# Performance work log

Hardware: AMD Instinct MI355X
Metric: run time of the kernel (lower is better)

## Reference

```python
import math
import jax, jax.numpy as jnp
import numpy as np

HIDDEN = 256
COND = 512
N_HEADS = 4


def _rope_freqs(seq_len, dim, theta=10000.0):
    inv = 1.0 / (theta ** (jnp.arange(0, dim, 2, dtype=jnp.float32) / dim))
    f = jnp.arange(seq_len, dtype=jnp.float32)[:, None] * inv[None, :]  # [t, dim/2]
    return jnp.concatenate([f, f], axis=-1)  # [t, dim]


def _rotate_half(x):
    x1, x2 = jnp.split(x, 2, axis=-1)
    return jnp.concatenate([-x2, x1], axis=-1)


def _apply_rope(pos, t):
    # pos: [T, c] broadcast over [b, h, T, c]
    return t * jnp.cos(pos) + _rotate_half(t) * jnp.sin(pos)


def _conv1(w, b, x):
    # 1x1 Conv1d: w [out, in], x [b, in, t]
    return jnp.einsum('oi,bit->bot', w, x) + b[None, :, None]


def setup_inputs() -> dict:
    key = jax.random.key(0)
    ks = jax.random.split(key, 12)
    B, Tt, Ts = 16, 2048, 512
    s = 0.02
    return {
        'x': jax.random.normal(ks[0], (B, HIDDEN, Tt), jnp.float32),
        'x_mask': jnp.ones((B, 1, Tt), jnp.float32),
        'cond_latent': jax.random.normal(ks[1], (B, COND, Ts), jnp.float32),
        'cond_mask': jnp.ones((B, 1, Ts), jnp.float32),
        'w_cond': jax.random.normal(ks[2], (HIDDEN, COND), jnp.float32) * s,
        'b_cond': jnp.zeros((HIDDEN,), jnp.float32),
        'wq': jax.random.normal(ks[3], (HIDDEN, HIDDEN), jnp.float32) * s,
        'bq': jnp.zeros((HIDDEN,), jnp.float32),
        'wk': jax.random.normal(ks[4], (HIDDEN, HIDDEN), jnp.float32) * s,
        'bk': jnp.zeros((HIDDEN,), jnp.float32),
        'wv': jax.random.normal(ks[5], (HIDDEN, HIDDEN), jnp.float32) * s,
        'bv': jnp.zeros((HIDDEN,), jnp.float32),
        'wo': jax.random.normal(ks[6], (HIDDEN, HIDDEN), jnp.float32) * s,
        'bo': jnp.zeros((HIDDEN,), jnp.float32),
        'w_film': jax.random.normal(ks[7], (2 * HIDDEN, HIDDEN), jnp.float32) * s,
        'b_film': jnp.zeros((2 * HIDDEN,), jnp.float32),
    }


def reference(x, x_mask, cond_latent, cond_mask,
              w_cond, b_cond, wq, bq, wk, bk, wv, bv, wo, bo, w_film, b_film):
    c = _conv1(w_cond, b_cond, cond_latent)          # [b, C, Ts]
    q = _conv1(wq, bq, x)                            # [b, C, Tt]
    k = _conv1(wk, bk, c)
    v = _conv1(wv, bv, c)

    B, C, Tt = q.shape
    Ts = k.shape[2]
    h = N_HEADS
    kc = C // h

    def split_heads(t):
        # [b, (h c), T] -> [b, h, T, c]
        return t.reshape(B, h, kc, t.shape[-1]).transpose(0, 1, 3, 2)

    q, k, v = split_heads(q), split_heads(k), split_heads(v)

    q = _apply_rope(_rope_freqs(Tt, kc), q)
    k = _apply_rope(_rope_freqs(Ts, kc), k)

    scores = jnp.einsum('bhtc,bhsc->bhts', q, k) / math.sqrt(kc)  # [b, h, Tt, Ts]
    attn_mask = cond_mask[:, :, None, :] * x_mask[:, :, :, None]  # [b, 1, Tt, Ts]
    scores = jnp.where(attn_mask == 0, jnp.float32(-1e4), scores)
    p = jax.nn.softmax(scores, axis=-1)  # dropout is identity at eval
    out = jnp.einsum('bhts,bhsc->bhtc', p, v)
    out = out.transpose(0, 1, 3, 2).reshape(B, C, Tt)  # [b, (h c), Tt]

    y = _conv1(wo, bo, out)                 # [b, C, Tt]
    gb = _conv1(w_film, b_film, y)          # [b, 2C, Tt]
    gamma, beta = jnp.split(gb, 2, axis=1)
    return (x * gamma + beta) * x_mask
```

## Files before the change

kernel.cpp:

```cpp
#include <hip/hip_runtime.h>
#include <math.h>

#define NB 16
#define CH 256
#define NH 4
#define KC 64
#define TTT 2048
#define TSS 512

typedef __attribute__((ext_vector_type(8))) short bf16x8;
typedef __attribute__((ext_vector_type(4))) float f32x4;

__device__ inline short f2bf(float x) {
  unsigned u = __float_as_uint(x);
  u += 0x7fffu + ((u >> 16) & 1u);
  return (short)(u >> 16);
}
__device__ inline unsigned pack2bf(float a, float b) {
  return (unsigned)(unsigned short)f2bf(a) | ((unsigned)(unsigned short)f2bf(b) << 16);
}

__device__ inline void fast_sincos_rev(float rev, float* sn, float* cs) {
  float fr = rev - truncf(rev);
#if __has_builtin(__builtin_amdgcn_sinf)
  *sn = __builtin_amdgcn_sinf(fr);
  *cs = __builtin_amdgcn_cosf(fr);
#else
  float ang = fr * 6.28318530717958648f;
  *sn = __sinf(ang);
  *cs = __cosf(ang);
#endif
}

#define INV2PI 0.15915494309189535f
#define ROPE_C 0.28782313662425572f

template <int TN, int NOUT>
__global__ __launch_bounds__(256) void gemm_v2(
    const float* __restrict__ W0, const float* __restrict__ b0,
    const float* __restrict__ W1, const float* __restrict__ b1,
    const float* __restrict__ X, float* __restrict__ Y0, float* __restrict__ Y1,
    int K, int T) {
  constexpr int TT = 16 * TN;
  constexpr int TQ = TT / 4;
  constexpr int PB = (32 * TQ) / 256;
  const int t0 = blockIdx.x * TT;
  const int m0 = blockIdx.y * 64;
  const int b  = blockIdx.z;
  const int tid = threadIdx.x;
  const int tx = tid & 15, ty = tid >> 4;

  __shared__ float As[NOUT][32][68];
  __shared__ float Bs[32][TT + 4];

  const float* Xb = X + (size_t)b * K * T;
  float acc[NOUT][4][TN];
#pragma unroll
  for (int n = 0; n < NOUT; ++n)
#pragma unroll
    for (int i = 0; i < 4; ++i)
#pragma unroll
      for (int u = 0; u < TN; ++u) acc[n][i][u] = 0.f;

  const int am = tid >> 2, akq = tid & 3;

  for (int k0 = 0; k0 < K; k0 += 32) {
#pragma unroll
    for (int n = 0; n < NOUT; ++n) {
      const float* Wn = (n == 0) ? W0 : W1;
      float4 a0 = *(const float4*)&Wn[(size_t)(m0 + am) * K + k0 + 4 * akq];
      float4 a1 = *(const float4*)&Wn[(size_t)(m0 + am) * K + k0 + 16 + 4 * akq];
      As[n][4 * akq + 0][am] = a0.x; As[n][4 * akq + 1][am] = a0.y;
      As[n][4 * akq + 2][am] = a0.z; As[n][4 * akq + 3][am] = a0.w;
      As[n][16 + 4 * akq + 0][am] = a1.x; As[n][16 + 4 * akq + 1][am] = a1.y;
      As[n][16 + 4 * akq + 2][am] = a1.z; As[n][16 + 4 * akq + 3][am] = a1.w;
    }
#pragma unroll
    for (int p = 0; p < PB; ++p) {
      int idx = tid + p * 256;
      int t4 = idx & (TQ - 1), k = idx / TQ;
      *(float4*)&Bs[k][4 * t4] = *(const float4*)&Xb[(size_t)(k0 + k) * T + t0 + 4 * t4];
    }
    __syncthreads();
#pragma unroll
    for (int kk = 0; kk < 32; ++kk) {
      float4 av[NOUT];
#pragma unroll
      for (int n = 0; n < NOUT; ++n) av[n] = *(const float4*)&As[n][kk][4 * ty];
      float4 bv[TN / 4];
#pragma unroll
      for (int g = 0; g < TN / 4; ++g) bv[g] = *(const float4*)&Bs[kk][4 * tx + 64 * g];
#pragma unroll
      for (int n = 0; n < NOUT; ++n) {
        const float a4[4] = {av[n].x, av[n].y, av[n].z, av[n].w};
#pragma unroll
        for (int i = 0; i < 4; ++i)
#pragma unroll
          for (int g = 0; g < TN / 4; ++g) {
            acc[n][i][4 * g + 0] += a4[i] * bv[g].x;
            acc[n][i][4 * g + 1] += a4[i] * bv[g].y;
            acc[n][i][4 * g + 2] += a4[i] * bv[g].z;
            acc[n][i][4 * g + 3] += a4[i] * bv[g].w;
          }
      }
    }
    __syncthreads();
  }
#pragma unroll
  for (int n = 0; n < NOUT; ++n) {
    float* Yn = (n == 0) ? Y0 : Y1;
    const float* bn = (n == 0) ? b0 : b1;
#pragma unroll
    for (int i = 0; i < 4; ++i) {
      int row = m0 + 4 * ty + i;
      float bi = bn[row];
#pragma unroll
      for (int g = 0; g < TN / 4; ++g) {
        float4 ov;
        ov.x = acc[n][i][4 * g + 0] + bi; ov.y = acc[n][i][4 * g + 1] + bi;
        ov.z = acc[n][i][4 * g + 2] + bi; ov.w = acc[n][i][4 * g + 3] + bi;
        *(float4*)&Yn[((size_t)b * 256 + row) * T + t0 + 4 * tx + 64 * g] = ov;
      }
    }
  }
}

__global__ __launch_bounds__(256, 2) void gemm_q_mfma(
    const short* __restrict__ wqbf, const float* __restrict__ bq,
    const float* __restrict__ X, short* __restrict__ qbf) {
  const int t0 = blockIdx.x * 64;
  const int b  = blockIdx.y;
  const int tid = threadIdx.x;
  const int w = tid >> 6, lane = tid & 63;
  const int quad = lane >> 4, l15 = lane & 15;

  __shared__ __align__(16) char smem[72704];
  float* Bsq = (float*)smem;
  float* Ep  = (float*)smem;

  const float* xb = X + (size_t)b * CH * TTT + t0;
#pragma unroll
  for (int p = 0; p < 16; ++p) {
    int idx = tid + p * 256;
    int t4 = idx & 15, k = idx >> 4;
    int swz = ((k >> 3) & 3) * 16;
    *(float4*)&Bsq[k * 68 + ((4 * t4) ^ swz)] =
        *(const float4*)&xb[(size_t)k * TTT + 4 * t4];
  }
  __syncthreads();

  const int mbase = w * 64;
  f32x4 acc[4][4];
#pragma unroll
  for (int mf = 0; mf < 4; ++mf)
#pragma unroll
    for (int nt = 0; nt < 4; ++nt) acc[mf][nt] = (f32x4){0.f, 0.f, 0.f, 0.f};

#pragma unroll
  for (int k0 = 0; k0 < 256; k0 += 32) {
    bf16x8 bfr[4];
#pragma unroll
    for (int nt = 0; nt < 4; ++nt) {
      int col = (nt * 16 + l15) ^ (quad * 16);
      bf16x8 f;
#pragma unroll
      for (int j = 0; j < 8; ++j)
        f[j] = f2bf(Bsq[(k0 + quad * 8 + j) * 68 + col]);
      bfr[nt] = f;
    }
#pragma unroll
    for (int mf = 0; mf < 4; ++mf) {
      bf16x8 af = *(const bf16x8*)&wqbf[(size_t)(mbase + mf * 16 + l15) * 256 + k0 + quad * 8];
#pragma unroll
      for (int nt = 0; nt < 4; ++nt)
        acc[mf][nt] = __builtin_amdgcn_mfma_f32_16x16x32_bf16(af, bfr[nt], acc[mf][nt], 0, 0, 0);
    }
  }
  __syncthreads();

#pragma unroll
  for (int mf = 0; mf < 4; ++mf)
#pragma unroll
    for (int r = 0; r < 4; ++r) {
      int row = mbase + mf * 16 + quad * 4 + r;
      float bi = bq[row];
#pragma unroll
      for (int nt = 0; nt < 4; ++nt)
        Ep[row * 71 + nt * 16 + l15] = acc[mf][nt][r] + bi;
    }
  __syncthreads();

  const int tt = tid >> 2, cb = tid & 3;
  float sn[8], cs[8];
  const float tg = (float)(t0 + tt);
#pragma unroll
  for (int e = 0; e < 8; ++e) {
    float invr = __expf(-(float)(cb * 8 + e) * ROPE_C) * INV2PI;
    fast_sincos_rev(tg * invr, &sn[e], &cs[e]);
  }
#pragma unroll
  for (int hh = 0; hh < 4; ++hh) {
    float oa[8], oc[8];
#pragma unroll
    for (int e = 0; e < 8; ++e) {
      int j = cb * 8 + e;
      float a = Ep[(hh * 64 + j) * 71 + tt];
      float c = Ep[(hh * 64 + j + 32) * 71 + tt];
      oa[e] = a * cs[e] - c * sn[e];
      oc[e] = c * cs[e] + a * sn[e];
    }
    short* dst = qbf + ((size_t)(b * NH + hh) * TTT + t0 + tt) * 64 + cb * 8;
    *(uint4*)dst = make_uint4(pack2bf(oa[0], oa[1]), pack2bf(oa[2], oa[3]),
                              pack2bf(oa[4], oa[5]), pack2bf(oa[6], oa[7]));
    *(uint4*)(dst + 32) = make_uint4(pack2bf(oc[0], oc[1]), pack2bf(oc[2], oc[3]),
                                     pack2bf(oc[4], oc[5]), pack2bf(oc[6], oc[7]));
  }
}

__global__ __launch_bounds__(256, 2) void gemm_kv_mfma(
    const short* __restrict__ wkvbf,
    const float* __restrict__ bk2, const float* __restrict__ bv2,
    const float* __restrict__ X, short* __restrict__ kbf, short* __restrict__ vbf) {
  const int t0 = blockIdx.x * 64;
  const int hh = blockIdx.y;
  const int b  = blockIdx.z;
  const int tid = threadIdx.x;
  const int w = tid >> 6, lane = tid & 63;
  const int quad = lane >> 4, l15 = lane & 15;

  __shared__ __align__(16) char smem[69632];
  short* Ls = (short*)smem;
  float* Kv = (float*)smem;

  const float* Xb = X + (size_t)b * 512 * TSS + t0;
#pragma unroll
  for (int p = 0; p < 32; ++p) {
    int idx = tid + p * 256;
    int s4 = idx & 15, k = idx >> 4;
    float4 v = *(const float4*)&Xb[(size_t)k * TSS + 4 * s4];
    uint2 w2 = make_uint2(pack2bf(v.x, v.y), pack2bf(v.z, v.w));
    *(uint2*)&Ls[k * 68 + 4 * s4] = w2;
  }
  __syncthreads();

  const int isV = w >> 1;
  const int wbase = (w & 1) * 32;
  const short* wbf = wkvbf + (size_t)(isV * 256 + hh * 64 + wbase) * 512;
  const float* bias = isV ? bv2 : bk2;

  f32x4 acc[2][4];
#pragma unroll
  for (int mf = 0; mf < 2; ++mf)
#pragma unroll
    for (int nt = 0; nt < 4; ++nt) acc[mf][nt] = (f32x4){0.f, 0.f, 0.f, 0.f};

#pragma unroll
  for (int k0 = 0; k0 < 512; k0 += 32) {
    bf16x8 bfr[4];
#pragma unroll
    for (int nt = 0; nt < 4; ++nt) {
      int s = nt * 16 + l15;
      bf16x8 f;
#pragma unroll
      for (int j = 0; j < 8; ++j)
        f[j] = Ls[(k0 + quad * 8 + j) * 68 + s];
      bfr[nt] = f;
    }
#pragma unroll
    for (int mf = 0; mf < 2; ++mf) {
      bf16x8 af = *(const bf16x8*)&wbf[(size_t)(mf * 16 + l15) * 512 + k0 + quad * 8];
#pragma unroll
      for (int nt = 0; nt < 4; ++nt)
        acc[mf][nt] = __builtin_amdgcn_mfma_f32_16x16x32_bf16(af, bfr[nt], acc[mf][nt], 0, 0, 0);
    }
  }
  __syncthreads();

#pragma unroll
  for (int mf = 0; mf < 2; ++mf)
#pragma unroll
    for (int r = 0; r < 4; ++r) {
      int lr = wbase + mf * 16 + quad * 4 + r;
      int ro = isV * 64 + lr;
      float bi = bias[hh * 64 + lr];
#pragma unroll
      for (int nt = 0; nt < 4; ++nt)
        Kv[ro * 68 + nt * 16 + l15] = acc[mf][nt][r] + bi;
    }
  __syncthreads();

  const int bh = b * NH + hh;

#pragma unroll
  for (int p = 0; p < 4; ++p) {
    int idx = tid + p * 256;
    int s4 = idx & 15, ch = idx >> 4;
    float4 v = *(const float4*)&Kv[(64 + ch) * 68 + 4 * s4];
    uint2 w2 = make_uint2(pack2bf(v.x, v.y), pack2bf(v.z, v.w));
    *(uint2*)&vbf[((size_t)bh * KC + ch) * TSS + t0 + 4 * s4] = w2;
  }

  {
    int s = tid >> 2, g = tid & 3;
    float sg = (float)(t0 + s);
    unsigned ow[8];
#pragma unroll
    for (int hlf = 0; hlf < 8; ++hlf) {
      int ch = g * 16 + hlf * 2;
      float o2[2];
#pragma unroll
      for (int q = 0; q < 2; ++q) {
        int c = ch + q;
        int j = c & 31;
        float invr = __expf(-(float)j * ROPE_C) * INV2PI;
        float snv, csv;
        fast_sincos_rev(sg * invr, &snv, &csv);
        float a = Kv[c * 68 + s];
        float pv = Kv[(c ^ 32) * 68 + s];
        o2[q] = (c < 32) ? (a * csv - pv * snv) : (a * csv + pv * snv);
      }
      ow[hlf] = pack2bf(o2[0], o2[1]);
    }
    short* dst = kbf + ((size_t)bh * TSS + t0 + s) * 64 + g * 16;
    *(uint4*)dst = make_uint4(ow[0], ow[1], ow[2], ow[3]);
    *(uint4*)(dst + 8) = make_uint4(ow[4], ow[5], ow[6], ow[7]);
  }
}

__global__ __launch_bounds__(256) void bias_fold(
    const float* __restrict__ wk, const float* __restrict__ bk,
    const float* __restrict__ wv, const float* __restrict__ bv,
    const float* __restrict__ bcond,
    const float* __restrict__ wfilm, const float* __restrict__ bo,
    const float* __restrict__ bfilm,
    float* __restrict__ bk2, float* __restrict__ bv2, float* __restrict__ bf2) {
  int g = blockIdx.x * 256 + threadIdx.x;
  if (g < 256) {
    float s = bk[g];
    for (int k = 0; k < 256; ++k) s += wk[g * 256 + k] * bcond[k];
    bk2[g] = s;
  } else if (g < 512) {
    int m = g - 256;
    float s = bv[m];
    for (int k = 0; k < 256; ++k) s += wv[m * 256 + k] * bcond[k];
    bv2[m] = s;
  } else if (g < 1024) {
    int m = g - 512;
    float s = bfilm[m];
    for (int k = 0; k < 256; ++k) s += wfilm[m * 256 + k] * bo[k];
    bf2[m] = s;
  }
}

__global__ __launch_bounds__(256) void cvt_bf16(
    const float* __restrict__ src, short* __restrict__ dst, int n) {
  int i = (blockIdx.x * 256 + threadIdx.x) * 8;
  if (i < n) {
    float4 a = *(const float4*)&src[i];
    float4 c = *(const float4*)&src[i + 4];
    uint4 w;
    w.x = pack2bf(a.x, a.y); w.y = pack2bf(a.z, a.w);
    w.z = pack2bf(c.x, c.y); w.w = pack2bf(c.z, c.w);
    *(uint4*)&dst[i] = w;
  }
}

__global__ __launch_bounds__(256, 3) void attn_mfma(
    const short* __restrict__ qbf, const short* __restrict__ kbf,
    const short* __restrict__ vbf, const float* __restrict__ cond_mask,
    short* __restrict__ obuf) {
  const int t0 = blockIdx.x * 64;
  const int h = blockIdx.y, b = blockIdx.z;
  const int bh = b * NH + h;
  const int tid = threadIdx.x;
  const int w = tid >> 6, lane = tid & 63;
  const int quad = lane >> 4, l15 = lane & 15;

  __shared__ __align__(16) char smem[49152];
  short* Ks = (short*)smem;
  short* Vs = (short*)(smem + 16384);
  short* Ps = (short*)(smem + 32768);

  const short* qb = qbf + ((size_t)bh * TTT + t0) * 64;
  const int trow_l = w * 16 + l15;
  bf16x8 qf0 = *(const bf16x8*)&qb[(size_t)trow_l * 64 + quad * 8];
  bf16x8 qf1 = *(const bf16x8*)&qb[(size_t)trow_l * 64 + 32 + quad * 8];

  f32x4 acc_o[4];
#pragma unroll
  for (int n = 0; n < 4; ++n) acc_o[n] = (f32x4){0.f, 0.f, 0.f, 0.f};
  float den[4] = {0.f, 0.f, 0.f, 0.f};

  const float* cm = cond_mask + (size_t)b * TSS;
  const short* kbase = kbf + (size_t)bh * TSS * 64;
  const short* vbase = vbf + (size_t)bh * KC * TSS;

  for (int s0 = 0; s0 < TSS; s0 += 128) {
    __syncthreads();
#pragma unroll
    for (int p = 0; p < 4; ++p) {
      int idx = tid + p * 256;
      int blk = idx & 7, sr = idx >> 3;
      *(uint4*)&Ks[sr * 64 + 8 * (blk ^ (sr & 7))] =
          *(const uint4*)&kbase[(size_t)(s0 + sr) * 64 + 8 * blk];
    }
#pragma unroll
    for (int p = 0; p < 4; ++p) {
      int idx = tid + p * 256;
      int blk = idx & 15, ch = idx >> 4;
      *(uint4*)&Vs[ch * 128 + 8 * (blk ^ (ch & 7))] =
          *(const uint4*)&vbase[(size_t)ch * TSS + s0 + 8 * blk];
    }
    __syncthreads();

#pragma unroll
    for (int n0 = 0; n0 < 8; ++n0) {
      int srow = n0 * 16 + l15;
      bf16x8 kf0 = *(const bf16x8*)&Ks[srow * 64 + 8 * (quad ^ (srow & 7))];
      bf16x8 kf1 = *(const bf16x8*)&Ks[srow * 64 + 8 * ((4 + quad) ^ (srow & 7))];
      f32x4 acc = (f32x4){0.f, 0.f, 0.f, 0.f};
      acc = __builtin_amdgcn_mfma_f32_16x16x32_bf16(qf0, kf0, acc, 0, 0, 0);
      acc = __builtin_amdgcn_mfma_f32_16x16x32_bf16(qf1, kf1, acc, 0, 0, 0);
      float mk = (cm[s0 + srow] != 0.f) ? 1.f : 0.f;
      int sblk = n0 * 2 + (l15 >> 3);
      int slow = l15 & 7;
#pragma unroll
      for (int r = 0; r < 4; ++r) {
        float e = __expf(acc[r] * 0.125f) * mk;
        den[r] += e;
        int trow = w * 16 + quad * 4 + r;
        Ps[trow * 128 + 8 * (sblk ^ (trow & 7)) + slow] = f2bf(e);
      }
    }

    {
      int trow = w * 16 + l15;
#pragma unroll
      for (int kt = 0; kt < 4; ++kt) {
        bf16x8 pf = *(const bf16x8*)&Ps[trow * 128 + 8 * ((kt * 4 + quad) ^ (trow & 7))];
#pragma unroll
        for (int n0 = 0; n0 < 4; ++n0) {
          int ch = n0 * 16 + l15;
          bf16x8 vf = *(const bf16x8*)&Vs[ch * 128 + 8 * ((kt * 4 + quad) ^ (ch & 7))];
          acc_o[n0] = __builtin_amdgcn_mfma_f32_16x16x32_bf16(pf, vf, acc_o[n0], 0, 0, 0);
        }
      }
    }
  }

  float rd[4];
#pragma unroll
  for (int r = 0; r < 4; ++r) {
    float d = den[r];
#pragma unroll
    for (int off = 1; off < 16; off <<= 1) d += __shfl_xor(d, off, 16);
    rd[r] = 1.f / fmaxf(d, 1e-30f);
  }

  __syncthreads();
  short* Os = (short*)smem;
#pragma unroll
  for (int n0 = 0; n0 < 4; ++n0)
#pragma unroll
    for (int r = 0; r < 4; ++r) {
      int ch = n0 * 16 + l15;
      int trow = w * 16 + quad * 4 + r;
      Os[trow * 64 + ch] = f2bf(acc_o[n0][r] * rd[r]);
    }
  __syncthreads();

  short* ob = obuf + ((size_t)b * TTT + t0) * CH + h * KC;
#pragma unroll
  for (int p = 0; p < 2; ++p) {
    int idx = tid + p * 256;
    int t = idx >> 3, c8 = idx & 7;
    *(uint4*)&ob[(size_t)t * CH + c8 * 8] = *(const uint4*)&Os[t * 64 + c8 * 8];
  }
}

__global__ __launch_bounds__(256) void film_mfma(
    const short* __restrict__ wfbf, const float* __restrict__ bf2,
    const short* __restrict__ ybf, const float* __restrict__ X,
    const float* __restrict__ xmask, float* __restrict__ out) {
  const int t0 = blockIdx.x * 64;
  const int b = blockIdx.y;
  const int tid = threadIdx.x;
  const int w = tid >> 6, lane = tid & 63;
  const int quad = lane >> 4, l15 = lane & 15;

  __shared__ __align__(16) short Ys[64 * 256];

  const short* yb = ybf + ((size_t)b * TTT + t0) * CH;
#pragma unroll
  for (int p = 0; p < 8; ++p) {
    int idx = tid + p * 256;
    int cb = idx & 31, tr = idx >> 5;
    *(uint4*)&Ys[tr * 256 + 8 * (cb ^ (tr & 7))] =
        *(const uint4*)&yb[(size_t)tr * CH + 8 * cb];
  }
  __syncthreads();

  const int mbase = w * 64;
  f32x4 accg[4][4], accb[4][4];
#pragma unroll
  for (int mf = 0; mf < 4; ++mf)
#pragma unroll
    for (int nt = 0; nt < 4; ++nt) {
      accg[mf][nt] = (f32x4){0.f, 0.f, 0.f, 0.f};
      accb[mf][nt] = (f32x4){0.f, 0.f, 0.f, 0.f};
    }

#pragma unroll
  for (int k0 = 0; k0 < 256; k0 += 32) {
    const int cb0 = (k0 >> 3) + quad;
    bf16x8 bfr[4];
#pragma unroll
    for (int nt = 0; nt < 4; ++nt) {
      int tr = nt * 16 + l15;
      bfr[nt] = *(const bf16x8*)&Ys[tr * 256 + 8 * (cb0 ^ (tr & 7))];
    }
#pragma unroll
    for (int mf = 0; mf < 4; ++mf) {
      int rowg = mbase + mf * 16 + l15;
      bf16x8 ag = *(const bf16x8*)&wfbf[(size_t)rowg * 256 + k0 + quad * 8];
      bf16x8 ab = *(const bf16x8*)&wfbf[(size_t)(256 + rowg) * 256 + k0 + quad * 8];
#pragma unroll
      for (int nt = 0; nt < 4; ++nt) {
        accg[mf][nt] = __builtin_amdgcn_mfma_f32_16x16x32_bf16(ag, bfr[nt], accg[mf][nt], 0, 0, 0);
        accb[mf][nt] = __builtin_amdgcn_mfma_f32_16x16x32_bf16(ab, bfr[nt], accb[mf][nt], 0, 0, 0);
      }
    }
  }

  const float* xb = X + (size_t)b * CH * TTT + t0;
  const float* xm = xmask + (size_t)b * TTT + t0;
  float* ob = out + (size_t)b * CH * TTT + t0;
  float xmv[4];
#pragma unroll
  for (int nt = 0; nt < 4; ++nt) xmv[nt] = xm[nt * 16 + l15];

#pragma unroll
  for (int mf = 0; mf < 4; ++mf) {
#pragma unroll
    for (int r = 0; r < 4; ++r) {
      int row = mbase + mf * 16 + quad * 4 + r;
      float bg = bf2[row];
      float bb = bf2[256 + row];
#pragma unroll
      for (int nt = 0; nt < 4; ++nt) {
        int t = nt * 16 + l15;
        float g  = accg[mf][nt][r] + bg;
        float bt = accb[mf][nt][r] + bb;
        float xv = xb[(size_t)row * TTT + t];
        ob[(size_t)row * TTT + t] = (xv * g + bt) * xmv[nt];
      }
    }
  }
}

extern "C" void kernel_launch(void* const* d_in, const int* in_sizes, int n_in,
                              void* d_out, int out_size, void* d_ws, size_t ws_size,
                              hipStream_t stream) {
  const float* x           = (const float*)d_in[0];
  const float* x_mask      = (const float*)d_in[1];
  const float* cond_latent = (const float*)d_in[2];
  const float* cond_mask   = (const float*)d_in[3];
  const float* w_cond      = (const float*)d_in[4];
  const float* b_cond      = (const float*)d_in[5];
  const float* wq          = (const float*)d_in[6];
  const float* bq          = (const float*)d_in[7];
  const float* wk          = (const float*)d_in[8];
  const float* bk          = (const float*)d_in[9];
  const float* wv          = (const float*)d_in[10];
  const float* bv          = (const float*)d_in[11];
  const float* wo          = (const float*)d_in[12];
  const float* bo          = (const float*)d_in[13];
  const float* w_film      = (const float*)d_in[14];
  const float* b_film      = (const float*)d_in[15];
  float* out = (float*)d_out;

  float* ws = (float*)d_ws;
  float* k_buf = ws;
  float* v_buf = k_buf + 2097152;
  float* wk2   = v_buf + 2097152;
  float* wv2   = wk2 + 131072;
  float* wf2   = wv2 + 131072;
  float* bk2   = wf2 + 131072;
  float* bv2   = bk2 + 256;
  float* bf2   = bv2 + 256;
  float* zbuf  = bf2 + 512;
  short* k_bf  = (short*)(zbuf + 512);
  short* v_bf  = k_bf + 2097152;
  short* wf2bf = v_bf + 2097152;
  short* q_bf  = wf2bf + 131072;
  short* wq_bf = q_bf + 8388608;
  short* wkv_bf = wq_bf + 65536;
  short* o_bf  = (short*)k_buf;

  dim3 blk(256);

  hipMemsetAsync(zbuf, 0, 512 * sizeof(float), stream);

  cvt_bf16<<<dim3(32), blk, 0, stream>>>(wq, wq_bf, 65536);
  gemm_v2<4, 2><<<dim3(8, 4, 1), blk, 0, stream>>>(
      wk, zbuf, wv, zbuf, w_cond, wk2, wv2, 256, 512);
  gemm_v2<4, 1><<<dim3(4, 8, 1), blk, 0, stream>>>(
      w_film, zbuf, nullptr, nullptr, wo, wf2, nullptr, 256, 256);
  cvt_bf16<<<dim3(128), blk, 0, stream>>>(wk2, wkv_bf, 262144);
  cvt_bf16<<<dim3(64), blk, 0, stream>>>(wf2, wf2bf, 131072);
  bias_fold<<<dim3(4), blk, 0, stream>>>(wk, bk, wv, bv, b_cond,
                                         w_film, bo, b_film, bk2, bv2, bf2);

  gemm_q_mfma<<<dim3(32, 16), blk, 0, stream>>>(wq_bf, bq, x, q_bf);
  gemm_kv_mfma<<<dim3(8, 4, 16), blk, 0, stream>>>(
      wkv_bf, bk2, bv2, cond_latent, k_bf, v_bf);
  attn_mfma<<<dim3(32, 4, 16), blk, 0, stream>>>(q_bf, k_bf, v_bf, cond_mask, o_bf);
  film_mfma<<<dim3(32, 16), blk, 0, stream>>>(wf2bf, bf2, o_bf, x, x_mask, out);
}
```

Measured before the change: 293.8 us.

## Halve Q-projection LDS with bf16 staging and write weight GEMMs as bf16

The Q projection kernel now converts x to bf16 while staging it into shared memory, which halves LDS use. The epilogue is split into two passes of 128 rows each so the smaller buffer still fits, and launch bounds rise to allow 4 blocks per CU. The weight-folding GEMMs now write bf16 directly, which removes two separate conversion kernels. The cost is an extra barrier phase in the epilogue and more register pressure under the higher occupancy target.

```diff
diff --git a/kernel.cpp b/kernel.cpp
--- a/kernel.cpp
+++ b/kernel.cpp
@@ -35,7 +35,7 @@
 #define INV2PI 0.15915494309189535f
 #define ROPE_C 0.28782313662425572f
 
-template <int TN, int NOUT>
+template <int TN, int NOUT, bool BF16OUT>
 __global__ __launch_bounds__(256) void gemm_v2(
     const float* __restrict__ W0, const float* __restrict__ b0,
     const float* __restrict__ W1, const float* __restrict__ b1,
@@ -116,16 +116,21 @@
       float bi = bn[row];
 #pragma unroll
       for (int g = 0; g < TN / 4; ++g) {
-        float4 ov;
-        ov.x = acc[n][i][4 * g + 0] + bi; ov.y = acc[n][i][4 * g + 1] + bi;
-        ov.z = acc[n][i][4 * g + 2] + bi; ov.w = acc[n][i][4 * g + 3] + bi;
-        *(float4*)&Yn[((size_t)b * 256 + row) * T + t0 + 4 * tx + 64 * g] = ov;
-      }
-    }
-  }
-}
-
-__global__ __launch_bounds__(256, 2) void gemm_q_mfma(
+        size_t oidx = ((size_t)b * 256 + row) * T + t0 + 4 * tx + 64 * g;
+        float ox = acc[n][i][4 * g + 0] + bi, oy = acc[n][i][4 * g + 1] + bi;
+        float oz = acc[n][i][4 * g + 2] + bi, ow = acc[n][i][4 * g + 3] + bi;
+        if (BF16OUT) {
+          uint2 w2 = make_uint2(pack2bf(ox, oy), pack2bf(oz, ow));
+          *(uint2*)&((short*)Yn)[oidx] = w2;
+        } else {
+          *(float4*)&Yn[oidx] = make_float4(ox, oy, oz, ow);
+        }
+      }
+    }
+  }
+}
+
+__global__ __launch_bounds__(256, 4) void gemm_q_mfma(
     const short* __restrict__ wqbf, const float* __restrict__ bq,
     const float* __restrict__ X, short* __restrict__ qbf) {
   const int t0 = blockIdx.x * 64;
@@ -134,8 +139,8 @@
   const int w = tid >> 6, lane = tid & 63;
   const int quad = lane >> 4, l15 = lane & 15;
 
-  __shared__ __align__(16) char smem[72704];
-  float* Bsq = (float*)smem;
+  __shared__ __align__(16) char smem[36352];
+  short* Bsq = (short*)smem;
   float* Ep  = (float*)smem;
 
   const float* xb = X + (size_t)b * CH * TTT + t0;
@@ -144,8 +149,9 @@
     int idx = tid + p * 256;
     int t4 = idx & 15, k = idx >> 4;
     int swz = ((k >> 3) & 3) * 16;
-    *(float4*)&Bsq[k * 68 + ((4 * t4) ^ swz)] =
-        *(const float4*)&xb[(size_t)k * TTT + 4 * t4];
+    float4 v = *(const float4*)&xb[(size_t)k * TTT + 4 * t4];
+    uint2 w2 = make_uint2(pack2bf(v.x, v.y), pack2bf(v.z, v.w));
+    *(uint2*)&Bsq[k * 68 + ((4 * t4) ^ swz)] = w2;
   }
   __syncthreads();
 
@@ -165,7 +171,7 @@
       bf16x8 f;
 #pragma unroll
       for (int j = 0; j < 8; ++j)
-        f[j] = f2bf(Bsq[(k0 + quad * 8 + j) * 68 + col]);
+        f[j] = Bsq[(k0 + quad * 8 + j) * 68 + col];
       bfr[nt] = f;
     }
 #pragma unroll
@@ -176,18 +182,6 @@
         acc[mf][nt] = __builtin_amdgcn_mfma_f32_16x16x32_bf16(af, bfr[nt], acc[mf][nt], 0, 0, 0);
     }
   }
-  __syncthreads();
-
-#pragma unroll
-  for (int mf = 0; mf < 4; ++mf)
-#pragma unroll
-    for (int r = 0; r < 4; ++r) {
-      int row = mbase + mf * 16 + quad * 4 + r;
-      float bi = bq[row];
-#pragma unroll
-      for (int nt = 0; nt < 4; ++nt)
-        Ep[row * 71 + nt * 16 + l15] = acc[mf][nt][r] + bi;
-    }
   __syncthreads();
 
   const int tt = tid >> 2, cb = tid & 3;
@@ -198,22 +192,42 @@
     float invr = __expf(-(float)(cb * 8 + e) * ROPE_C) * INV2PI;
     fast_sincos_rev(tg * invr, &sn[e], &cs[e]);
   }
-#pragma unroll
-  for (int hh = 0; hh < 4; ++hh) {
-    float oa[8], oc[8];
-#pragma unroll
-    for (int e = 0; e < 8; ++e) {
-      int j = cb * 8 + e;
-      float a = Ep[(hh * 64 + j) * 71 + tt];
-      float c = Ep[(hh * 64 + j + 32) * 71 + tt];
-      oa[e] = a * cs[e] - c * sn[e];
-      oc[e] = c * cs[e] + a * sn[e];
-    }
-    short* dst = qbf + ((size_t)(b * NH + hh) * TTT + t0 + tt) * 64 + cb * 8;
-    *(uint4*)dst = make_uint4(pack2bf(oa[0], oa[1]), pack2bf(oa[2], oa[3]),
-                              pack2bf(oa[4], oa[5]), pack2bf(oa[6], oa[7]));
-    *(uint4*)(dst + 32) = make_uint4(pack2bf(oc[0], oc[1]), pack2bf(oc[2], oc[3]),
-                                     pack2bf(oc[4], oc[5]), pack2bf(oc[6], oc[7]));
+
+#pragma unroll
+  for (int pp = 0; pp < 2; ++pp) {
+    if ((w >> 1) == pp) {
+#pragma unroll
+      for (int mf = 0; mf < 4; ++mf)
+#pragma unroll
+        for (int r = 0; r < 4; ++r) {
+          int mrow = mf * 16 + quad * 4 + r;
+          int lrow = (w & 1) * 64 + mrow;
+          float bi = bq[mbase + mrow];
+#pragma unroll
+          for (int nt = 0; nt < 4; ++nt)
+            Ep[lrow * 71 + nt * 16 + l15] = acc[mf][nt][r] + bi;
+        }
+    }
+    __syncthreads();
+#pragma unroll
+    for (int hl = 0; hl < 2; ++hl) {
+      int hh = pp * 2 + hl;
+      float oa[8], oc[8];
+#pragma unroll
+      for (int e = 0; e < 8; ++e) {
+        int j = cb * 8 + e;
+        float a = Ep[(hl * 64 + j) * 71 + tt];
+        float c = Ep[(hl * 64 + j + 32) * 71 + tt];
+        oa[e] = a * cs[e] - c * sn[e];
+        oc[e] = c * cs[e] + a * sn[e];
+      }
+      short* dst = qbf + ((size_t)(b * NH + hh) * TTT + t0 + tt) * 64 + cb * 8;
+      *(uint4*)dst = make_uint4(pack2bf(oa[0], oa[1]), pack2bf(oa[2], oa[3]),
+                                pack2bf(oa[4], oa[5]), pack2bf(oa[6], oa[7]));
+      *(uint4*)(dst + 32) = make_uint4(pack2bf(oc[0], oc[1]), pack2bf(oc[2], oc[3]),
+                                       pack2bf(oc[4], oc[5]), pack2bf(oc[6], oc[7]));
+    }
+    if (pp == 0) __syncthreads();
   }
 }
 
@@ -602,12 +616,10 @@
   hipMemsetAsync(zbuf, 0, 512 * sizeof(float), stream);
 
   cvt_bf16<<<dim3(32), blk, 0, stream>>>(wq, wq_bf, 65536);
-  gemm_v2<4, 2><<<dim3(8, 4, 1), blk, 0, stream>>>(
-      wk, zbuf, wv, zbuf, w_cond, wk2, wv2, 256, 512);
-  gemm_v2<4, 1><<<dim3(4, 8, 1), blk, 0, stream>>>(
-      w_film, zbuf, nullptr, nullptr, wo, wf2, nullptr, 256, 256);
-  cvt_bf16<<<dim3(128), blk, 0, stream>>>(wk2, wkv_bf, 262144);
-  cvt_bf16<<<dim3(64), blk, 0, stream>>>(wf2, wf2bf, 131072);
+  gemm_v2<4, 2, true><<<dim3(8, 4, 1), blk, 0, stream>>>(
+      wk, zbuf, wv, zbuf, w_cond, (float*)wkv_bf, (float*)(wkv_bf + 131072), 256, 512);
+  gemm_v2<4, 1, true><<<dim3(4, 8, 1), blk, 0, stream>>>(
+      w_film, zbuf, nullptr, nullptr, wo, (float*)wf2bf, nullptr, 256, 256);
   bias_fold<<<dim3(4), blk, 0, stream>>>(wk, bk, wv, bv, b_cond,
                                          w_film, bo, b_film, bk2, bv2, bf2);
 
```

Measured after the change: 303.5 us. 3.3% more time.
